# Kernel optimization log

Hardware: AMD Instinct MI355X
Metric: run time of the kernel (lower is better)

Reference implementation:

```python
import jax, jax.numpy as jnp
import numpy as np

N_HEADS = 32
N_KV_HEADS = 8
HEAD_DIM = 128
DIM = 4096
BSZ = 2
SEQLEN = 2048
ROPE_THETA = 500000.0


def setup_inputs() -> dict:
    key = jax.random.key(0)
    ks = jax.random.split(key, 6)
    s = 0.02
    x = jax.random.normal(ks[0], (BSZ, SEQLEN, DIM), dtype=jnp.float32)
    wq = jax.random.normal(ks[1], (N_HEADS * HEAD_DIM, DIM), dtype=jnp.float32) * s
    wk = jax.random.normal(ks[2], (N_KV_HEADS * HEAD_DIM, DIM), dtype=jnp.float32) * s
    wv = jax.random.normal(ks[3], (N_KV_HEADS * HEAD_DIM, DIM), dtype=jnp.float32) * s
    wo = jax.random.normal(ks[4], (DIM, N_HEADS * HEAD_DIM), dtype=jnp.float32) * s
    cache_k = jnp.zeros((BSZ, SEQLEN, N_KV_HEADS, HEAD_DIM), dtype=jnp.float32)
    cache_v = jnp.zeros((BSZ, SEQLEN, N_KV_HEADS, HEAD_DIM), dtype=jnp.float32)
    # rotary frequencies: freqs_cis[t, j] = exp(i * t * theta^(-2j/hd)); pass cos/sin parts
    inv = 1.0 / (ROPE_THETA ** (jnp.arange(0, HEAD_DIM, 2, dtype=jnp.float32) / HEAD_DIM))
    t = jnp.arange(SEQLEN, dtype=jnp.float32)
    ang = jnp.outer(t, inv)  # [S, hd/2]
    freqs_cos = jnp.cos(ang)
    freqs_sin = jnp.sin(ang)
    # causal additive mask
    mask = jnp.triu(jnp.full((SEQLEN, SEQLEN), -jnp.inf, dtype=jnp.float32), k=1)
    return {"x": x, "wq": wq, "wk": wk, "wv": wv, "wo": wo,
            "cache_k": cache_k, "cache_v": cache_v,
            "freqs_cos": freqs_cos, "freqs_sin": freqs_sin,
            "mask": mask, "start_pos": 0}


def _apply_rope(t, cos, sin):
    # t: [B, S, h, hd]; cos/sin: [S, hd/2]
    B, S, h, hd = t.shape
    tf = t.astype(jnp.float32).reshape(B, S, h, hd // 2, 2)
    a, b = tf[..., 0], tf[..., 1]
    c = cos[None, :, None, :]
    s = sin[None, :, None, :]
    out = jnp.stack([a * c - b * s, a * s + b * c], axis=-1)
    return out.reshape(B, S, h, hd).astype(t.dtype)


def reference(x, wq, wk, wv, wo, cache_k, cache_v, freqs_cos, freqs_sin, mask, start_pos):
    B, S, D = x.shape
    hd = HEAD_DIM
    n_rep = N_HEADS // N_KV_HEADS
    xq = (x @ wq.T).reshape(B, S, N_HEADS, hd)
    xk = (x @ wk.T).reshape(B, S, N_KV_HEADS, hd)
    xv = (x @ wv.T).reshape(B, S, N_KV_HEADS, hd)
    xq = _apply_rope(xq, freqs_cos, freqs_sin)
    xk = _apply_rope(xk, freqs_cos, freqs_sin)
    # KV cache write + slice
    cache_k = jax.lax.dynamic_update_slice(cache_k, xk, (0, start_pos, 0, 0))
    cache_v = jax.lax.dynamic_update_slice(cache_v, xv, (0, start_pos, 0, 0))
    kv_len = start_pos + S
    keys = cache_k[:B, :kv_len]    # [B, K, kvh, hd]
    values = cache_v[:B, :kv_len]
    # GQA: repeat kv heads
    keys = jnp.repeat(keys, n_rep, axis=2)     # [B, K, H, hd]
    values = jnp.repeat(values, n_rep, axis=2)
    q = xq.transpose(0, 2, 1, 3)       # [B, H, S, hd]
    k = keys.transpose(0, 2, 1, 3)     # [B, H, K, hd]
    v = values.transpose(0, 2, 1, 3)
    scores = jnp.einsum('bhqd,bhkd->bhqk', q, k) / jnp.sqrt(jnp.float32(hd))
    if mask is not None:
        scores = scores + mask[None, None, :, :]
    probs = jax.nn.softmax(scores.astype(jnp.float32), axis=-1).astype(q.dtype)
    out = jnp.einsum('bhqk,bhkd->bhqd', probs, v)
    out = out.transpose(0, 2, 1, 3).reshape(B, S, N_HEADS * hd)
    return out @ wo.T
```

## Files before the change

### kernel.cpp

```cpp
#include <hip/hip_runtime.h>
#include <hip/hip_bf16.h>
#include <math.h>

typedef __attribute__((ext_vector_type(8)))  __bf16 bfrag;
typedef __attribute__((ext_vector_type(4)))  float  f32x4;
typedef __attribute__((ext_vector_type(16))) float  f32x16;
typedef __attribute__((ext_vector_type(8)))  short  s16x8;
typedef __attribute__((ext_vector_type(4)))  short  s16x4;
typedef __attribute__((ext_vector_type(2)))  unsigned u32x2;
typedef __attribute__((ext_vector_type(4)))  unsigned u32x4;

__device__ __forceinline__ short f2bf(float f) {
  return (short)__builtin_bit_cast(unsigned short, (__bf16)f);
}
__device__ __forceinline__ float bf2f(short s) {
  return (float)__builtin_bit_cast(__bf16, (unsigned short)s);
}
__device__ __forceinline__ unsigned cvtpk(float lo, float hi_) {
  unsigned r;
  asm("v_cvt_pk_bf16_f32 %0, %1, %2" : "=v"(r) : "v"(lo), "v"(hi_));
  return r;
}
__device__ __forceinline__ void gll16(const void* g, void* l) {
  __builtin_amdgcn_global_load_lds((const __attribute__((address_space(1))) void*)g,
                                   (__attribute__((address_space(3))) void*)l, 16, 0, 0);
}

__global__ __launch_bounds__(256) void cvt_f32_bf16(const float* __restrict__ in,
                                                    short* __restrict__ out, int n4) {
  int i = blockIdx.x * 256 + threadIdx.x;
  if (i >= n4) return;
  f32x4 v = __builtin_nontemporal_load((const f32x4*)in + i);
  s16x4 o;
  o.x = f2bf(v.x); o.y = f2bf(v.y); o.z = f2bf(v.z); o.w = f2bf(v.w);
  ((s16x4*)out)[i] = o;
}

__global__ __launch_bounds__(256) void cvt4(const float* __restrict__ x,
                                            const float* __restrict__ wq,
                                            const float* __restrict__ wk,
                                            const float* __restrict__ wv,
                                            short* __restrict__ xb,
                                            short* __restrict__ wqb,
                                            short* __restrict__ wkb,
                                            short* __restrict__ wvb) {
  const int b = blockIdx.x;
  const float* in; short* out; int base;
  if (b < 16384)      { in = x;  out = xb;  base = 0; }
  else if (b < 32768) { in = wq; out = wqb; base = 16384 * 256; }
  else if (b < 36864) { in = wk; out = wkb; base = 32768 * 256; }
  else                { in = wv; out = wvb; base = 36864 * 256; }
  const int idx = b * 256 + threadIdx.x - base;
  f32x4 v = __builtin_nontemporal_load((const f32x4*)in + idx);
  s16x4 o;
  o.x = f2bf(v.x); o.y = f2bf(v.y); o.z = f2bf(v.z); o.w = f2bf(v.w);
  ((s16x4*)out)[idx] = o;
}

#define STG_(OP, OPs, boff, bb, hh, kt_, Kd)                                     \
  do {                                                                           \
    _Pragma("unroll")                                                            \
    for (int s = 0; s < 2; ++s)                                                  \
      gll16(OP + (size_t)(boff + (hh) * 128 + s * 64 + r0) * Kd + (kt_) * 64 + csrc * 8, \
            (char*)OPs[bb] + ((hh) * 128 + s * 64 + wid * 8) * 128);             \
  } while (0)

template<bool ROPE>
__global__ __launch_bounds__(512) void gemm128n(const short* __restrict__ A,
                                                const short* __restrict__ B,
                                                short* __restrict__ C,
                                                short* __restrict__ vt,
                                                int M, int N, int K, int NBX,
                                                const float* __restrict__ fcos,
                                                const float* __restrict__ fsin) {
  __shared__ __align__(16) short As[2][128 * 64];
  __shared__ __align__(16) short Bs[2][256 * 64];
  const int tid = threadIdx.x, lane = tid & 63, wid = tid >> 6;
  const int lr = lane & 15, lg = lane >> 4;
  const int wm = wid >> 2, wn = wid & 3;
  const int orig = blockIdx.x;
  const int xc = orig & 7, o8 = orig >> 3;
  const int s8 = o8 >> 5, t8 = o8 & 31;
  const int bmi = ((xc >> 1) << 3) + (t8 >> 2);
  const int bni = (xc & 1) * (NBX >> 1) + (s8 << 2) + (t8 & 3);
  const int bm = bmi << 7, bn = bni << 8;
  const int NT = K >> 6;
  const int r0 = tid >> 3;
  const int c0 = tid & 7;
  const int csrc = c0 ^ (r0 & 7);

  int ch[2];
#pragma unroll
  for (int ks = 0; ks < 2; ++ks) ch[ks] = (((ks << 2) | lg) ^ (lr & 7)) << 4;
  const int aoff  = (wm * 64 + lr) * 128;
  const int boff2 = (wn * 32 + lr) * 128;

#define RD_A(dst, bb)                                                            \
  do {                                                                           \
    const char* ab = (const char*)As[bb] + aoff;                                 \
    _Pragma("unroll") for (int i = 0; i < 4; ++i)                                \
      _Pragma("unroll") for (int ks = 0; ks < 2; ++ks)                           \
        dst[i][ks] = *(const bfrag*)(ab + i * 2048 + ch[ks]);                    \
  } while (0)
#define RD_B(dst, bb, jh)                                                        \
  do {                                                                           \
    const char* bp = (const char*)Bs[bb] + boff2 + (jh) * 16384;                 \
    _Pragma("unroll") for (int j = 0; j < 2; ++j)                                \
      _Pragma("unroll") for (int ks = 0; ks < 2; ++ks)                           \
        dst[j][ks] = *(const bfrag*)(bp + j * 2048 + ch[ks]);                    \
  } while (0)
#define MFMA16(af, bf, jh)                                                       \
  do {                                                                           \
    __builtin_amdgcn_s_setprio(1);                                               \
    _Pragma("unroll") for (int ks = 0; ks < 2; ++ks)                             \
      _Pragma("unroll") for (int i = 0; i < 4; ++i)                              \
        _Pragma("unroll") for (int j = 0; j < 2; ++j)                            \
          acc[i][(jh) * 2 + j] = __builtin_amdgcn_mfma_f32_16x16x32_bf16(        \
              af[i][ks], bf[j][ks], acc[i][(jh) * 2 + j], 0, 0, 0);              \
    __builtin_amdgcn_s_setprio(0);                                               \
  } while (0)

  STG_(A, As, bm, 0, 0, 0, K);
  STG_(B, Bs, bn, 0, 0, 0, K);
  STG_(B, Bs, bn, 0, 1, 0, K);
  if (NT > 1) {
    STG_(A, As, bm, 1, 0, 1, K);
    STG_(B, Bs, bn, 1, 0, 1, K);
    asm volatile("s_waitcnt vmcnt(4)" ::: "memory");
  } else {
    asm volatile("s_waitcnt vmcnt(0)" ::: "memory");
  }
  __builtin_amdgcn_s_barrier();
  __builtin_amdgcn_sched_barrier(0);

  f32x4 acc[4][4] = {};
  bfrag a_[4][2], b_lo[2][2], b_hi[2][2];

  for (int kt = 0; kt < NT; ++kt) {
    const int b = kt & 1;
    RD_A(a_, b);
    RD_B(b_lo, b, 0);
    if (kt + 1 < NT) STG_(B, Bs, bn, b ^ 1, 1, kt + 1, K);
    MFMA16(a_, b_lo, 0);
    __builtin_amdgcn_s_barrier();
    __builtin_amdgcn_sched_barrier(0);
    RD_B(b_hi, b, 1);
    if (kt + 2 < NT) {
      STG_(A, As, bm, b, 0, kt + 2, K);
      STG_(B, Bs, bn, b, 0, kt + 2, K);
    }
    MFMA16(a_, b_hi, 1);
    if (kt + 1 < NT) {
      if (kt + 2 < NT) asm volatile("s_waitcnt vmcnt(4)" ::: "memory");
      else             asm volatile("s_waitcnt vmcnt(0)" ::: "memory");
      __builtin_amdgcn_s_barrier();
      __builtin_amdgcn_sched_barrier(0);
    }
  }
#undef RD_A
#undef RD_B
#undef MFMA16
  const int rb = bm + wm * 64 + lg * 4, cb = bn + wn * 32 + lr;
  if (ROPE && bn < 5120) {
    const bool odd = (lr & 1) != 0;
#pragma unroll
    for (int j = 0; j < 2; ++j) {
      const int iidx = (wn * 32 + j * 16 + lr) >> 1;
#pragma unroll
      for (int i = 0; i < 4; ++i)
#pragma unroll
        for (int r = 0; r < 4; ++r) {
          const int row = rb + i * 16 + r;
          const int sp = row & 2047;
          const float c  = fcos[sp * 64 + iidx];
          const float sn = fsin[sp * 64 + iidx];
#pragma unroll
          for (int jh = 0; jh < 2; ++jh) {
            float own = acc[i][jh * 2 + j][r];
            float par = __shfl_xor(own, 1, 64);
            float out = odd ? (par * sn + own * c) : (own * c - par * sn);
            C[(size_t)row * N + (cb + jh * 128 + j * 16)] = f2bf(out);
          }
        }
    }
  } else if (ROPE) {
#pragma unroll
    for (int jh = 0; jh < 2; ++jh)
#pragma unroll
      for (int j = 0; j < 2; ++j) {
        const int vcol = cb + jh * 128 + j * 16 - 5120;
        const int kvh = vcol >> 7, d = vcol & 127;
#pragma unroll
        for (int i = 0; i < 4; ++i) {
          const int row0 = rb + i * 16;
          const int bb = row0 >> 11, s0 = row0 & 2047;
          s16x4 v;
#pragma unroll
          for (int r = 0; r < 4; ++r) v[r] = f2bf(acc[i][jh * 2 + j][r]);
          *(s16x4*)(vt + (size_t)((bb * 8 + kvh) * 128 + d) * 2048 + s0) = v;
        }
      }
  } else {
#pragma unroll
    for (int i = 0; i < 4; ++i)
#pragma unroll
      for (int jh = 0; jh < 2; ++jh)
#pragma unroll
        for (int j = 0; j < 2; ++j)
#pragma unroll
          for (int r = 0; r < 4; ++r)
            C[(size_t)(rb + i * 16 + r) * N + (cb + jh * 128 + j * 16)] =
                f2bf(acc[i][jh * 2 + j][r]);
  }
}

template<bool BF16OUT>
__global__ __launch_bounds__(512) void gemm256p(const short* __restrict__ A,
                                                const short* __restrict__ B,
                                                void* __restrict__ Cv,
                                                int M, int N, int K, int NBX) {
  __shared__ __align__(16) short As[2][256 * 64];
  __shared__ __align__(16) short Bs[2][256 * 64];
  const int tid = threadIdx.x, lane = tid & 63, wid = tid >> 6;
  const int lr = lane & 15, lg = lane >> 4;
  const int wm = wid >> 2, wn = wid & 3;
  const int orig = blockIdx.x;
  const int xc = orig & 7, o8 = orig >> 3;
  const int bmi = ((xc >> 1) << 2) + (o8 & 3);
  const int bni = (xc & 1) * (NBX >> 1) + (o8 >> 2);
  const int bm = bmi << 8, bn = bni << 8;
  const int NT = K >> 6;
  const int r0 = tid >> 3;
  const int c0 = tid & 7;
  const int csrc = c0 ^ (r0 & 7);

  int ch[2];
#pragma unroll
  for (int ks = 0; ks < 2; ++ks) ch[ks] = (((ks << 2) | lg) ^ (lr & 7)) << 4;
  const int aoff = (wm * 128 + lr) * 128;
  const int boff = (wn * 64 + lr) * 128;

#define RD_A8(dst, bb, ih)                                                       \
  do {                                                                           \
    const char* ab = (const char*)As[bb] + aoff + (ih) * 8192;                   \
    _Pragma("unroll") for (int i = 0; i < 4; ++i)                                \
      _Pragma("unroll") for (int ks = 0; ks < 2; ++ks)                           \
        dst[i][ks] = *(const bfrag*)(ab + i * 2048 + ch[ks]);                    \
  } while (0)
#define RD_B4(dst, bb, jh)                                                       \
  do {                                                                           \
    const char* bp = (const char*)Bs[bb] + boff + (jh) * 4096;                   \
    _Pragma("unroll") for (int j = 0; j < 2; ++j)                                \
      _Pragma("unroll") for (int ks = 0; ks < 2; ++ks)                           \
        dst[j][ks] = *(const bfrag*)(bp + j * 2048 + ch[ks]);                    \
  } while (0)
#define QUAD(af, bf, ih, jh)                                                     \
  do {                                                                           \
    __builtin_amdgcn_s_setprio(1);                                               \
    _Pragma("unroll") for (int ks = 0; ks < 2; ++ks)                             \
      _Pragma("unroll") for (int i = 0; i < 4; ++i)                              \
        _Pragma("unroll") for (int j = 0; j < 2; ++j)                            \
          acc[(ih) * 4 + i][(jh) * 2 + j] = __builtin_amdgcn_mfma_f32_16x16x32_bf16( \
              af[i][ks], bf[j][ks], acc[(ih) * 4 + i][(jh) * 2 + j], 0, 0, 0);   \
    __builtin_amdgcn_s_setprio(0);                                               \
  } while (0)
#define BARRIER() do { __builtin_amdgcn_s_barrier(); __builtin_amdgcn_sched_barrier(0); } while (0)

  STG_(A, As, bm, 0, 0, 0, K); STG_(A, As, bm, 0, 1, 0, K);
  STG_(B, Bs, bn, 0, 0, 0, K); STG_(B, Bs, bn, 0, 1, 0, K);
  STG_(B, Bs, bn, 1, 0, 1, K); STG_(B, Bs, bn, 1, 1, 1, K);
  asm volatile("s_waitcnt vmcnt(4)" ::: "memory");
  BARRIER();

  f32x4 acc[8][4] = {};
  bfrag a_[4][2], b_lo[2][2], b_hi[2][2];
  const int NI = NT >> 1;

  for (int it = 0; it < NI; ++it) {
    const int O  = 2 * it + 1;
    int E2 = 2 * it + 2; if (E2 >= NT) E2 = 0;
    int O2 = 2 * it + 3; if (O2 >= NT) O2 = 0;
    RD_A8(a_, 0, 0);
    RD_B4(b_lo, 0, 0);
    STG_(A, As, bm, 1, 0, O, K);
    BARRIER();
    asm volatile("s_waitcnt lgkmcnt(0)" ::: "memory");
    QUAD(a_, b_lo, 0, 0);
    BARRIER();
    RD_B4(b_hi, 0, 1);
    STG_(A, As, bm, 1, 1, O, K);
    BARRIER();
    asm volatile("s_waitcnt lgkmcnt(0)" ::: "memory");
    QUAD(a_, b_hi, 0, 1);
    BARRIER();
    RD_A8(a_, 0, 1);
    STG_(B, Bs, bn, 0, 0, E2, K);
    BARRIER();
    asm volatile("s_waitcnt lgkmcnt(0)" ::: "memory");
    QUAD(a_, b_hi, 1, 1);
    BARRIER();
    STG_(B, Bs, bn, 0, 1, E2, K);
    asm volatile("s_waitcnt vmcnt(4)" ::: "memory");
    BARRIER();
    QUAD(a_, b_lo, 1, 0);
    BARRIER();
    RD_A8(a_, 1, 0);
    RD_B4(b_lo, 1, 0);
    STG_(A, As, bm, 0, 0, E2, K);
    BARRIER();
    asm volatile("s_waitcnt lgkmcnt(0)" ::: "memory");
    QUAD(a_, b_lo, 0, 0);
    BARRIER();
    RD_B4(b_hi, 1, 1);
    STG_(A, As, bm, 0, 1, E2, K);
    BARRIER();
    asm volatile("s_waitcnt lgkmcnt(0)" ::: "memory");
    QUAD(a_, b_hi, 0, 1);
    BARRIER();
    RD_A8(a_, 1, 1);
    STG_(B, Bs, bn, 1, 0, O2, K);
    BARRIER();
    asm volatile("s_waitcnt lgkmcnt(0)" ::: "memory");
    QUAD(a_, b_hi, 1, 1);
    BARRIER();
    STG_(B, Bs, bn, 1, 1, O2, K);
    asm volatile("s_waitcnt vmcnt(4)" ::: "memory");
    BARRIER();
    QUAD(a_, b_lo, 1, 0);
    BARRIER();
  }
#undef RD_A8
#undef RD_B4
#undef QUAD
#undef BARRIER
  const int rb = bm + wm * 128 + lg * 4, cb = bn + wn * 64 + lr;
#pragma unroll
  for (int i = 0; i < 8; ++i)
#pragma unroll
    for (int j = 0; j < 4; ++j)
#pragma unroll
      for (int r = 0; r < 4; ++r) {
        size_t idx = (size_t)(rb + i * 16 + r) * N + (cb + j * 16);
        if (BF16OUT) ((short*)Cv)[idx] = f2bf(acc[i][j][r]);
        else         ((float*)Cv)[idx] = acc[i][j][r];
      }
}

__global__ __launch_bounds__(512, 2) void fattn2(const short* __restrict__ qkv,
                                                 const short* __restrict__ vt,
                                                 short* __restrict__ ao) {
  const int b = blockIdx.z, h = blockIdx.y;
  const int qb = b ? (int)gridDim.x - 1 - blockIdx.x : blockIdx.x;
  const int kvh = h >> 2;
  const int tid = threadIdx.x;
  const int lane = tid & 63, wid = tid >> 6;
  const int l31 = lane & 31, hi = lane >> 5;
  __shared__ __align__(16) short Ks[2][64 * 128];
  __shared__ __align__(16) short Vs[2][128 * 64];

  const int q0w   = qb * 256 + wid * 32;
  const int qg    = q0w + l31;
  const int tmaxw = q0w >> 6;
  const int NT    = 4 * qb + 4;

  bfrag qf[8];
  {
    const short* qp = qkv + (size_t)(b * 2048 + qg) * 6144 + h * 128 + hi * 8;
#pragma unroll
    for (int kk = 0; kk < 8; ++kk) qf[kk] = *(const bfrag*)(qp + kk * 16);
  }

  const int kr0 = tid >> 4, kcc = tid & 15;
  const int vd0 = tid >> 3, vkc = tid & 7;
  const int kro[2] = { kr0, kr0 + 32 };
  const int vdo[2] = { vd0, vd0 + 64 };
  int kldst[2], vldst[2];
#pragma unroll
  for (int i = 0; i < 2; ++i) {
    kldst[i] = (kro[i] * 256 + kcc * 16) ^ ((kro[i] & 7) << 4);
    vldst[i] = (vdo[i] * 128 + vkc * 16) ^ ((vdo[i] & 7) << 4);
  }
  const short* base_k = qkv + (size_t)(b * 2048) * 6144 + 4096 + kvh * 128;
  const short* base_v = vt + (size_t)((b * 8 + kvh) * 128) * 2048;

  {
    s16x8 kr_[2], vr_[2];
#pragma unroll
    for (int i = 0; i < 2; ++i) {
      kr_[i] = *(const s16x8*)(base_k + (size_t)kro[i] * 6144 + kcc * 8);
      vr_[i] = *(const s16x8*)(base_v + (size_t)vdo[i] * 2048 + vkc * 8);
    }
#pragma unroll
    for (int i = 0; i < 2; ++i) {
      *(s16x8*)((char*)Ks[0] + kldst[i]) = kr_[i];
      *(s16x8*)((char*)Vs[0] + vldst[i]) = vr_[i];
    }
  }
  __syncthreads();

  f32x16 o[4] = {};
  float m = -3.0e38f, l = 0.f;
  const float c0 = 0.08838834764831845f * 1.4426950408889634f;
  const int  sw = (l31 & 7) << 4;

  for (int t = 0; t < NT; ++t) {
    const int cur = t & 1;
    s16x8 kr_[2], vr_[2];
    const bool pf = (t + 1 < NT);
    if (pf) {
#pragma unroll
      for (int i = 0; i < 2; ++i) {
        kr_[i] = *(const s16x8*)(base_k + (size_t)((t + 1) * 64 + kro[i]) * 6144 + kcc * 8);
        vr_[i] = *(const s16x8*)(base_v + (size_t)vdo[i] * 2048 + (t + 1) * 64 + vkc * 8);
      }
    }
    if (t <= tmaxw) {
      f32x16 st[2] = {};
      {
        const char* kb = (const char*)Ks[cur] + l31 * 256;
        __builtin_amdgcn_s_setprio(1);
#pragma unroll
        for (int kk = 0; kk < 8; ++kk) {
          const int ko = (kk * 32 + hi * 16) ^ sw;
          bfrag kf0 = *(const bfrag*)(kb + ko);
          bfrag kf1 = *(const bfrag*)(kb + 8192 + ko);
          st[0] = __builtin_amdgcn_mfma_f32_32x32x16_bf16(kf0, qf[kk], st[0], 0, 0, 0);
          st[1] = __builtin_amdgcn_mfma_f32_32x32x16_bf16(kf1, qf[kk], st[1], 0, 0, 0);
        }
        __builtin_amdgcn_s_setprio(0);
      }
      if (t == tmaxw) {
        const int kb0 = t * 64 + 4 * hi;
#pragma unroll
        for (int kt = 0; kt < 2; ++kt)
#pragma unroll
          for (int r = 0; r < 16; ++r) {
            int k = kb0 + kt * 32 + (r & 3) + 8 * (r >> 2);
            if (k > qg) st[kt][r] = -3.0e38f;
          }
      }
      float mt = -3.0e38f;
#pragma unroll
      for (int kt = 0; kt < 2; ++kt)
#pragma unroll
        for (int r = 0; r < 16; ++r) mt = fmaxf(mt, st[kt][r]);
      mt = fmaxf(mt, __shfl_xor(mt, 32, 64));
      if (!__all((mt - m) * c0 <= 8.0f)) {
        float nm = fmaxf(m, mt);
        float fe = exp2f((m - nm) * c0);
        m = nm;
        l *= fe;
#pragma unroll
        for (int dt = 0; dt < 4; ++dt)
#pragma unroll
          for (int r = 0; r < 16; ++r) o[dt][r] *= fe;
      }
      const float mc = m * c0;
      float ps = 0.f;
#pragma unroll
      for (int kt = 0; kt < 2; ++kt)
#pragma unroll
        for (int r = 0; r < 16; ++r) {
          float p = exp2f(st[kt][r] * c0 - mc);
          st[kt][r] = p;
          ps += p;
        }
      ps += __shfl_xor(ps, 32, 64);
      l += ps;
      bfrag pfr[4];
#pragma unroll
      for (int kt = 0; kt < 2; ++kt) {
        u32x2 a0 = __builtin_amdgcn_permlane32_swap(cvtpk(st[kt][0],  st[kt][1]),
                                                    cvtpk(st[kt][4],  st[kt][5]),  0, 0);
        u32x2 a1 = __builtin_amdgcn_permlane32_swap(cvtpk(st[kt][2],  st[kt][3]),
                                                    cvtpk(st[kt][6],  st[kt][7]),  0, 0);
        u32x2 b0 = __builtin_amdgcn_permlane32_swap(cvtpk(st[kt][8],  st[kt][9]),
                                                    cvtpk(st[kt][12], st[kt][13]), 0, 0);
        u32x2 b1 = __builtin_amdgcn_permlane32_swap(cvtpk(st[kt][10], st[kt][11]),
                                                    cvtpk(st[kt][14], st[kt][15]), 0, 0);
        u32x4 w0 = { a0.x, a1.x, a0.y, a1.y };
        u32x4 w1 = { b0.x, b1.x, b0.y, b1.y };
        pfr[kt * 2]     = __builtin_bit_cast(bfrag, w0);
        pfr[kt * 2 + 1] = __builtin_bit_cast(bfrag, w1);
      }
      __builtin_amdgcn_s_setprio(1);
#pragma unroll
      for (int ks = 0; ks < 4; ++ks) {
        const char* vb = (const char*)Vs[cur] + l31 * 128 + ((ks * 32 + hi * 16) ^ sw);
#pragma unroll
        for (int dt = 0; dt < 4; ++dt) {
          bfrag vf = *(const bfrag*)(vb + dt * 4096);
          o[dt] = __builtin_amdgcn_mfma_f32_32x32x16_bf16(vf, pfr[ks], o[dt], 0, 0, 0);
        }
      }
      __builtin_amdgcn_s_setprio(0);
    }
    __syncthreads();
    if (pf) {
#pragma unroll
      for (int i = 0; i < 2; ++i) {
        *(s16x8*)((char*)Ks[cur ^ 1] + kldst[i]) = kr_[i];
        *(s16x8*)((char*)Vs[cur ^ 1] + vldst[i]) = vr_[i];
      }
    }
    __syncthreads();
  }
  const float linv = 1.f / l;
  short* aop = ao + (size_t)(b * 2048 + qg) * 4096 + h * 128 + 4 * hi;
#pragma unroll
  for (int dt = 0; dt < 4; ++dt)
#pragma unroll
    for (int r = 0; r < 16; ++r) {
      int d = dt * 32 + (r & 3) + 8 * (r >> 2);
      aop[d] = f2bf(o[dt][r] * linv);
    }
}

extern "C" void kernel_launch(void* const* d_in, const int* in_sizes, int n_in,
                              void* d_out, int out_size, void* d_ws, size_t ws_size,
                              hipStream_t stream) {
  const float* x  = (const float*)d_in[0];
  const float* wq = (const float*)d_in[1];
  const float* wk = (const float*)d_in[2];
  const float* wv = (const float*)d_in[3];
  const float* wo = (const float*)d_in[4];
  const float* fc = (const float*)d_in[7];
  const float* fs = (const float*)d_in[8];

  char* ws = (char*)d_ws;
  short* xb    = (short*)(ws);
  short* ao    = xb;
  short* wqkvb = (short*)(ws + 33554432ull);
  short* qkv   = (short*)(ws + 83886080ull);
  short* vt    = (short*)(ws + 134217728ull);
  short* wob   = (short*)(ws + 167772160ull);

  cvt4<<<40960, 256, 0, stream>>>(x, wq, wk, wv,
                                  xb, wqkvb, wqkvb + 16777216, wqkvb + 20971520);
  gemm128n<true><<<768, 512, 0, stream>>>(xb, wqkvb, qkv, vt,
                                          4096, 6144, 4096, 24, fc, fs);
  cvt_f32_bf16<<<16384, 256, 0, stream>>>(wo, wob, 4194304);
  fattn2<<<dim3(8, 32, 2), 512, 0, stream>>>(qkv, vt, ao);
  gemm256p<false><<<256, 512, 0, stream>>>(ao, wob, (float*)d_out, 4096, 4096, 4096, 16);
}
```

Baseline: 477.5 us.

## Split QKV projection into 256-tile Q GEMM and 128x256 KV GEMM

Moves the Q part of the QKV projection (first 4096 output columns) onto the larger 256x256-tile gemm256p kernel, with RoPE fused into its epilogue. The K/V columns stay on gemm128n, which now takes a parameter for where V starts and uses offset pointers. The aim is better data reuse and efficiency on the bulk of the projection. The cost is an extra kernel launch, and the 256 blocks of the K/V GEMM alone may underfill the device.

```diff
diff --git a/kernel.cpp b/kernel.cpp
--- a/kernel.cpp
+++ b/kernel.cpp
@@ -70,7 +70,7 @@
                                                 const short* __restrict__ B,
                                                 short* __restrict__ C,
                                                 short* __restrict__ vt,
-                                                int M, int N, int K, int NBX,
+                                                int M, int N, int K, int NBX, int vstart,
                                                 const float* __restrict__ fcos,
                                                 const float* __restrict__ fsin) {
   __shared__ __align__(16) short As[2][128 * 64];
@@ -161,7 +161,7 @@
 #undef RD_B
 #undef MFMA16
   const int rb = bm + wm * 64 + lg * 4, cb = bn + wn * 32 + lr;
-  if (ROPE && bn < 5120) {
+  if (ROPE && bn < vstart) {
     const bool odd = (lr & 1) != 0;
 #pragma unroll
     for (int j = 0; j < 2; ++j) {
@@ -188,7 +188,7 @@
     for (int jh = 0; jh < 2; ++jh)
 #pragma unroll
       for (int j = 0; j < 2; ++j) {
-        const int vcol = cb + jh * 128 + j * 16 - 5120;
+        const int vcol = cb + jh * 128 + j * 16 - vstart;
         const int kvh = vcol >> 7, d = vcol & 127;
 #pragma unroll
         for (int i = 0; i < 4; ++i) {
@@ -214,11 +214,13 @@
   }
 }
 
-template<bool BF16OUT>
+template<int OMODE>
 __global__ __launch_bounds__(512) void gemm256p(const short* __restrict__ A,
                                                 const short* __restrict__ B,
                                                 void* __restrict__ Cv,
-                                                int M, int N, int K, int NBX) {
+                                                int M, int N, int K, int NBX,
+                                                const float* __restrict__ fcos,
+                                                const float* __restrict__ fsin) {
   __shared__ __align__(16) short As[2][256 * 64];
   __shared__ __align__(16) short Bs[2][256 * 64];
   const int tid = threadIdx.x, lane = tid & 63, wid = tid >> 6;
@@ -334,16 +336,34 @@
 #undef QUAD
 #undef BARRIER
   const int rb = bm + wm * 128 + lg * 4, cb = bn + wn * 64 + lr;
-#pragma unroll
-  for (int i = 0; i < 8; ++i)
-#pragma unroll
-    for (int j = 0; j < 4; ++j)
-#pragma unroll
-      for (int r = 0; r < 4; ++r) {
-        size_t idx = (size_t)(rb + i * 16 + r) * N + (cb + j * 16);
-        if (BF16OUT) ((short*)Cv)[idx] = f2bf(acc[i][j][r]);
-        else         ((float*)Cv)[idx] = acc[i][j][r];
-      }
+  if (OMODE == 1) {
+    const bool odd = (lr & 1) != 0;
+#pragma unroll
+    for (int j = 0; j < 4; ++j) {
+      const int iidx = ((wn * 64 + j * 16 + lr) & 127) >> 1;
+#pragma unroll
+      for (int i = 0; i < 8; ++i)
+#pragma unroll
+        for (int r = 0; r < 4; ++r) {
+          const int row = rb + i * 16 + r;
+          const int sp = row & 2047;
+          const float c  = fcos[sp * 64 + iidx];
+          const float sn = fsin[sp * 64 + iidx];
+          float own = acc[i][j][r];
+          float par = __shfl_xor(own, 1, 64);
+          float out = odd ? (par * sn + own * c) : (own * c - par * sn);
+          ((short*)Cv)[(size_t)row * N + (cb + j * 16)] = f2bf(out);
+        }
+    }
+  } else {
+#pragma unroll
+    for (int i = 0; i < 8; ++i)
+#pragma unroll
+      for (int j = 0; j < 4; ++j)
+#pragma unroll
+        for (int r = 0; r < 4; ++r)
+          ((float*)Cv)[(size_t)(rb + i * 16 + r) * N + (cb + j * 16)] = acc[i][j][r];
+  }
 }
 
 __global__ __launch_bounds__(512, 2) void fattn2(const short* __restrict__ qkv,
@@ -537,9 +557,11 @@
 
   cvt4<<<40960, 256, 0, stream>>>(x, wq, wk, wv,
                                   xb, wqkvb, wqkvb + 16777216, wqkvb + 20971520);
-  gemm128n<true><<<768, 512, 0, stream>>>(xb, wqkvb, qkv, vt,
-                                          4096, 6144, 4096, 24, fc, fs);
+  gemm256p<1><<<256, 512, 0, stream>>>(xb, wqkvb, qkv, 4096, 6144, 4096, 16, fc, fs);
+  gemm128n<true><<<256, 512, 0, stream>>>(xb, wqkvb + 16777216ull, qkv + 4096, vt,
+                                          4096, 6144, 4096, 8, 1024, fc, fs);
   cvt_f32_bf16<<<16384, 256, 0, stream>>>(wo, wob, 4194304);
   fattn2<<<dim3(8, 32, 2), 512, 0, stream>>>(qkv, vt, ao);
-  gemm256p<false><<<256, 512, 0, stream>>>(ao, wob, (float*)d_out, 4096, 4096, 4096, 16);
-}
+  gemm256p<0><<<256, 512, 0, stream>>>(ao, wob, (float*)d_out, 4096, 4096, 4096, 16,
+                                       nullptr, nullptr);
+}
```

New measurement: 471.2 us. Within noise of the previous version (-1.3%).
